# Performance work log

Measured on AMD Instinct MI355X. Metric: run time of the kernel, lower is better.

Reference implementation:

```python
import jax, jax.numpy as jnp
import numpy as np

EMBED = 768
HIDDEN = 3072
HEADS = 12
EPS = 1e-6


def _ln(x, g, b):
    mu = jnp.mean(x, axis=-1, keepdims=True)
    var = jnp.mean(jnp.square(x - mu), axis=-1, keepdims=True)
    return (x - mu) / jnp.sqrt(var + EPS) * g + b


def setup_inputs() -> dict:
    key = jax.random.key(0)
    ks = jax.random.split(key, 12)
    s = lambda fan_in: 1.0 / np.sqrt(fan_in)
    x = jax.random.normal(ks[0], (16, 1024, EMBED), dtype=jnp.float32)
    return {
        "x": x,
        "ln1_g": jnp.ones((EMBED,), jnp.float32),
        "ln1_b": jnp.zeros((EMBED,), jnp.float32),
        "qkv_w": jax.random.uniform(ks[1], (3 * EMBED, EMBED), jnp.float32, -s(EMBED), s(EMBED)),
        "qkv_b": jax.random.uniform(ks[2], (3 * EMBED,), jnp.float32, -s(EMBED), s(EMBED)),
        "proj_w": jax.random.uniform(ks[3], (EMBED, EMBED), jnp.float32, -s(EMBED), s(EMBED)),
        "proj_b": jax.random.uniform(ks[4], (EMBED,), jnp.float32, -s(EMBED), s(EMBED)),
        "ln2_g": jnp.ones((EMBED,), jnp.float32),
        "ln2_b": jnp.zeros((EMBED,), jnp.float32),
        "fc1_w": jax.random.uniform(ks[5], (HIDDEN, EMBED), jnp.float32, -s(EMBED), s(EMBED)),
        "fc1_b": jax.random.uniform(ks[6], (HIDDEN,), jnp.float32, -s(EMBED), s(EMBED)),
        "fc2_w": jax.random.uniform(ks[7], (EMBED, HIDDEN), jnp.float32, -s(HIDDEN), s(HIDDEN)),
        "fc2_b": jax.random.uniform(ks[8], (EMBED,), jnp.float32, -s(HIDDEN), s(HIDDEN)),
    }


def reference(x, ln1_g, ln1_b, qkv_w, qkv_b, proj_w, proj_b, ln2_g, ln2_b, fc1_w, fc1_b, fc2_w, fc2_b):
    B, N, D = x.shape
    Hd = D // HEADS
    scale = Hd ** -0.5
    # attention branch
    xn = _ln(x, ln1_g, ln1_b)
    qkv = xn @ qkv_w.T + qkv_b  # [B,N,3D]
    qkv = qkv.reshape(B, N, 3, HEADS, Hd).transpose(2, 0, 3, 1, 4)
    q, k, v = qkv[0], qkv[1], qkv[2]  # [B,H,N,Hd]
    attn = jax.nn.softmax(jnp.einsum("bhqd,bhkd->bhqk", q, k) * scale, axis=-1)
    ctx = jnp.einsum("bhqk,bhkd->bhqd", attn, v)
    ctx = ctx.transpose(0, 2, 1, 3).reshape(B, N, D)
    x = x + ctx @ proj_w.T + proj_b
    # MLP branch
    h = _ln(x, ln2_g, ln2_b)
    h = jax.nn.gelu(h @ fc1_w.T + fc1_b, approximate=False)
    x = x + h @ fc2_w.T + fc2_b
    return x
```

## Files before the change

kernel.cpp:

```cpp
#include <hip/hip_runtime.h>
#include <math.h>


typedef unsigned short u16;
typedef __attribute__((ext_vector_type(8))) short bf16x8;
typedef __attribute__((ext_vector_type(4))) float f32x4;

#define MFMA_BF16(a, b, c) __builtin_amdgcn_mfma_f32_16x16x32_bf16((a), (b), (c), 0, 0, 0)
#define WAITV(N) asm volatile("s_waitcnt vmcnt(" #N ")" ::: "memory")
#define WAITLGKM0 asm volatile("s_waitcnt lgkmcnt(0)" ::: "memory")
#define SCHED0 __builtin_amdgcn_sched_barrier(0)
#define EXP2F(x) __builtin_amdgcn_exp2f(x)

#define QSCALE 0.18033688011112042f
#define C8LOG2E 11.541560327111707f

__device__ __forceinline__ float bf2f(u16 v) {
    return __uint_as_float(((unsigned)v) << 16);
}
__device__ __forceinline__ u16 f2bf(float f) {
    unsigned u = __float_as_uint(f);
    u += 0x7fffu + ((u >> 16) & 1u);
    return (u16)(u >> 16);
}
__device__ __forceinline__ unsigned cvtpk_bf16(float lo, float hi) {
    unsigned r;
    asm volatile("v_cvt_pk_bf16_f32 %0, %1, %2" : "=v"(r) : "v"(lo), "v"(hi));
    return r;
}

__device__ __forceinline__ float gelu_fast(float v) {
    const float t = v * v;
    const float z = v * (1.5957691216f + 0.0713548162f * t);
    const float e = __expf(-z);
    return v * __builtin_amdgcn_rcpf(1.0f + e);
}

typedef __attribute__((address_space(1))) const void gvoid;
typedef __attribute__((address_space(3))) void lvoid;
__device__ __forceinline__ void gll16(const void* g, void* l) {
    __builtin_amdgcn_global_load_lds((gvoid*)g, (lvoid*)l, 16, 0, 0);
}

__global__ __launch_bounds__(256) void cast32(const float* __restrict__ src,
                                              u16* __restrict__ dst, int n8) {
    const int i = blockIdx.x * 256 + threadIdx.x;
    if (i >= n8) return;
    const float4 a = ((const float4*)src)[2 * i];
    const float4 b = ((const float4*)src)[2 * i + 1];
    bf16x8 r;
    r[0] = (short)f2bf(a.x); r[1] = (short)f2bf(a.y);
    r[2] = (short)f2bf(a.z); r[3] = (short)f2bf(a.w);
    r[4] = (short)f2bf(b.x); r[5] = (short)f2bf(b.y);
    r[6] = (short)f2bf(b.z); r[7] = (short)f2bf(b.w);
    ((bf16x8*)dst)[i] = r;
}

__global__ __launch_bounds__(256) void ln_kernel(const float* __restrict__ x,
                                                 const float* __restrict__ g,
                                                 const float* __restrict__ b,
                                                 u16* __restrict__ out) {
    const int row = blockIdx.x;
    const int t = threadIdx.x;
    const float* xr = x + (size_t)row * 768;
    float v0 = xr[t], v1 = xr[t + 256], v2 = xr[t + 512];
    float s = v0 + v1 + v2;
    float sq = v0 * v0 + v1 * v1 + v2 * v2;
#pragma unroll
    for (int off = 32; off > 0; off >>= 1) {
        s += __shfl_down(s, off);
        sq += __shfl_down(sq, off);
    }
    __shared__ float red_s[4], red_sq[4], sh_mu, sh_rs;
    const int wave = t >> 6, lane = t & 63;
    if (lane == 0) { red_s[wave] = s; red_sq[wave] = sq; }
    __syncthreads();
    if (t == 0) {
        float S = red_s[0] + red_s[1] + red_s[2] + red_s[3];
        float SQ = red_sq[0] + red_sq[1] + red_sq[2] + red_sq[3];
        float mu = S * (1.0f / 768.0f);
        float var = SQ * (1.0f / 768.0f) - mu * mu;
        sh_mu = mu;
        sh_rs = 1.0f / sqrtf(fmaxf(var, 0.0f) + 1e-6f);
    }
    __syncthreads();
    const float mu = sh_mu, rs = sh_rs;
    u16* orow = out + (size_t)row * 768;
    orow[t]       = f2bf((v0 - mu) * rs * g[t]       + b[t]);
    orow[t + 256] = f2bf((v1 - mu) * rs * g[t + 256] + b[t + 256]);
    orow[t + 512] = f2bf((v2 - mu) * rs * g[t + 512] + b[t + 512]);
}

template <int EPI, int BF16B>
__global__ __launch_bounds__(256, 2) void gemm2(
        const u16* __restrict__ A, const void* __restrict__ Bv,
        const float* __restrict__ bias, const float* __restrict__ res,
        void* __restrict__ Cv, u16* __restrict__ vtb, int N, int K) {
    __shared__ __align__(16) u16 As[128 * 32];
    __shared__ __align__(16) u16 Bs[128 * 32];
    const int t = threadIdx.x;
    const int wave = t >> 6, lane = t & 63;
    const int quad = lane >> 4, mr = lane & 15;
    const int wm = wave >> 1, wn = wave & 1;
    const int m0 = blockIdx.y * 128;
    const int n0 = blockIdx.x * 128;

    f32x4 acc[4][4];
#pragma unroll
    for (int i = 0; i < 4; i++)
#pragma unroll
        for (int j = 0; j < 4; j++) acc[i][j] = (f32x4){0.f, 0.f, 0.f, 0.f};

    const int seg = wave * 2;
    const int drow = lane >> 2;
    const int dcol = (lane & 3) * 8;
    const int sr = t >> 2, skv = t & 3;

    for (int k0 = 0; k0 < K; k0 += 32) {
#pragma unroll
        for (int c = 0; c < 2; c++) {
            const int rowA = (seg + c) * 16 + drow;
            gll16(A + (size_t)(m0 + rowA) * K + k0 + dcol, &As[(seg + c) * 512]);
        }
        if (BF16B) {
            const u16* Bh = (const u16*)Bv;
#pragma unroll
            for (int c = 0; c < 2; c++) {
                const int rowB = (seg + c) * 16 + drow;
                gll16(Bh + (size_t)(n0 + rowB) * K + k0 + dcol, &Bs[(seg + c) * 512]);
            }
        } else {
            const float* Bf = (const float*)Bv;
#pragma unroll
            for (int half = 0; half < 2; half++) {
                const float* src = Bf + (size_t)(n0 + sr + half * 64) * K + k0 + skv * 8;
                const float4 a = *(const float4*)src;
                const float4 b2 = *(const float4*)(src + 4);
                bf16x8 r;
                r[0] = (short)f2bf(a.x);  r[1] = (short)f2bf(a.y);
                r[2] = (short)f2bf(a.z);  r[3] = (short)f2bf(a.w);
                r[4] = (short)f2bf(b2.x); r[5] = (short)f2bf(b2.y);
                r[6] = (short)f2bf(b2.z); r[7] = (short)f2bf(b2.w);
                *(bf16x8*)&Bs[(sr + half * 64) * 32 + skv * 8] = r;
            }
        }
        __syncthreads();
        bf16x8 af[4], bfr[4];
#pragma unroll
        for (int i = 0; i < 4; i++)
            af[i] = *(const bf16x8*)&As[(wm * 64 + i * 16 + mr) * 32 + quad * 8];
#pragma unroll
        for (int j = 0; j < 4; j++)
            bfr[j] = *(const bf16x8*)&Bs[(wn * 64 + j * 16 + mr) * 32 + quad * 8];
#pragma unroll
        for (int i = 0; i < 4; i++)
#pragma unroll
            for (int j = 0; j < 4; j++)
                acc[i][j] = MFMA_BF16(af[i], bfr[j], acc[i][j]);
        __syncthreads();
    }

#pragma unroll
    for (int i = 0; i < 4; i++) {
#pragma unroll
        for (int r = 0; r < 4; r++) {
            const int m = m0 + wm * 64 + i * 16 + quad * 4 + r;
#pragma unroll
            for (int j = 0; j < 4; j++) {
                const int n = n0 + wn * 64 + j * 16 + mr;
                float v = acc[i][j][r] + bias[n];
                if (EPI == 1) {
                    v = gelu_fast(v);
                    ((u16*)Cv)[(size_t)m * N + n] = f2bf(v);
                } else if (EPI == 2) {
                    v += res[(size_t)m * N + n];
                    ((float*)Cv)[(size_t)m * N + n] = v;
                } else {
                    if (n < 1536) {
                        const float vq = (n < 768) ? v * QSCALE : v;
                        ((u16*)Cv)[(size_t)m * 1536 + n] = f2bf(vq);
                    } else {
                        const int h = (n - 1536) >> 6, hd = (n - 1536) & 63;
                        const int bb = m >> 10, pos = m & 1023;
                        vtb[((size_t)(bb * 12 + h) * 64 + hd) * 1024 + pos] = f2bf(v);
                    }
                }
            }
        }
    }
}

#define AFRAG(T, ROW, KS) \
    (*(const bf16x8*)&(T)[(ROW)][(((((KS) << 2) | quad)) ^ ((ROW) & 7)) << 3])

#define ACCUM(ACCEL, AF, BF)                                  \
    do {                                                      \
        if (EPI == 3) (ACCEL) = MFMA_BF16((AF), (BF), (ACCEL)); \
        else          (ACCEL) = MFMA_BF16((BF), (AF), (ACCEL)); \
    } while (0)

template <int EPI, int NSLOT>
__global__ __launch_bounds__(512, 2) void gemm8(
        const u16* __restrict__ A, const u16* __restrict__ Bw,
        const float* __restrict__ bias, const float* __restrict__ res,
        void* __restrict__ Cv, u16* __restrict__ vtb, int N, int K) {
    constexpr int TN = NSLOT * 64;
    __shared__ __align__(16) u16 SMEM[(512 + 2 * TN) * 64];
    u16(&As)[2][256][64] = *reinterpret_cast<u16(*)[2][256][64]>(&SMEM[0]);
    u16(&Bs)[2][TN][64] = *reinterpret_cast<u16(*)[2][TN][64]>(&SMEM[512 * 64]);
    const int t = threadIdx.x;
    const int wave = t >> 6, lane = t & 63;
    const int quad = lane >> 4, mr = lane & 15;
    const int wm = wave >> 2, wn = wave & 3;
    const int gx = gridDim.x;
    const int nwg = gx * gridDim.y;
    int bid = blockIdx.y * gx + blockIdx.x;
    bid = (bid & 7) * (nwg >> 3) + (bid >> 3);
    const int m0 = (bid / gx) * 256, n0 = (bid % gx) * TN;
    const int NT = K >> 6;

    const int srow = wave * 8 + (lane >> 3);
    const int sgrp = ((lane & 7) ^ (lane >> 3)) * 8;

    const u16* Abase = A + (size_t)(m0 + srow) * K + sgrp;
    const u16* Bbase = Bw + (size_t)(n0 + srow) * K + sgrp;

#define STAGE_A(BI, SLOT, KT) \
    gll16(Abase + ((size_t)(SLOT) * 64) * K + (KT) * 64, &As[BI][(SLOT) * 64 + wave * 8][0])
#define STAGE_B(BI, SLOT, KT) \
    gll16(Bbase + ((size_t)(SLOT) * 64) * K + (KT) * 64, &Bs[BI][(SLOT) * 64 + wave * 8][0])

    STAGE_A(0, 0, 0); STAGE_A(0, 1, 0); STAGE_A(0, 2, 0); STAGE_A(0, 3, 0);
#pragma unroll
    for (int s = 0; s < NSLOT; s++) STAGE_B(0, s, 0);
    if (NT > 1) { STAGE_A(1, 0, 1); STAGE_A(1, 2, 1); STAGE_B(1, 0, 1); STAGE_B(1, 1, 1); }

    f32x4 acc[8][NSLOT];
#pragma unroll
    for (int i = 0; i < 8; i++)
#pragma unroll
        for (int j = 0; j < NSLOT; j++) acc[i][j] = (f32x4){0.f, 0.f, 0.f, 0.f};

    if (NT > 1) { WAITV(4); } else { WAITV(0); }
    __builtin_amdgcn_s_barrier();
    SCHED0;

    for (int kt = 0; kt < NT; ++kt) {
        const int bi = kt & 1;
        const u16(*Ab)[64] = As[bi];
        const u16(*Bb)[64] = Bs[bi];
        const bool st1 = (kt + 1 < NT);
        const bool st2 = (kt + 2 < NT);

        if (st1) {
#pragma unroll
            for (int s = 2; s < NSLOT; s++) STAGE_B(bi ^ 1, s, kt + 1);
            STAGE_A(bi ^ 1, 1, kt + 1); STAGE_A(bi ^ 1, 3, kt + 1);
        }

        bf16x8 af[4], bfv[NSLOT];
#pragma unroll
        for (int j = 0; j < NSLOT; j++) bfv[j] = AFRAG(Bb, wn * (NSLOT * 16) + j * 16 + mr, 0);
#pragma unroll
        for (int i = 0; i < 4; i++) af[i] = AFRAG(Ab, wm * 128 + i * 16 + mr, 0);
#pragma unroll
        for (int i = 0; i < 4; i++)
#pragma unroll
            for (int j = 0; j < NSLOT; j++) ACCUM(acc[i][j], af[i], bfv[j]);
#pragma unroll
        for (int i = 0; i < 4; i++) af[i] = AFRAG(Ab, wm * 128 + 64 + i * 16 + mr, 0);
#pragma unroll
        for (int i = 0; i < 4; i++)
#pragma unroll
            for (int j = 0; j < NSLOT; j++) ACCUM(acc[4 + i][j], af[i], bfv[j]);
#pragma unroll
        for (int j = 0; j < NSLOT; j++) bfv[j] = AFRAG(Bb, wn * (NSLOT * 16) + j * 16 + mr, 1);
#pragma unroll
        for (int i = 0; i < 4; i++) af[i] = AFRAG(Ab, wm * 128 + i * 16 + mr, 1);
#pragma unroll
        for (int i = 0; i < 4; i++)
#pragma unroll
            for (int j = 0; j < NSLOT; j++) ACCUM(acc[i][j], af[i], bfv[j]);
#pragma unroll
        for (int i = 0; i < 4; i++) af[i] = AFRAG(Ab, wm * 128 + 64 + i * 16 + mr, 1);
#pragma unroll
        for (int i = 0; i < 4; i++)
#pragma unroll
            for (int j = 0; j < NSLOT; j++) ACCUM(acc[4 + i][j], af[i], bfv[j]);

        WAITLGKM0;
        SCHED0;
        __builtin_amdgcn_s_barrier();
        SCHED0;
        if (st2) { STAGE_A(bi, 0, kt + 2); STAGE_A(bi, 2, kt + 2);
                   STAGE_B(bi, 0, kt + 2); STAGE_B(bi, 1, kt + 2); }
        SCHED0;
        if (st2) { WAITV(4); } else { WAITV(0); }
        __builtin_amdgcn_s_barrier();
        SCHED0;
    }

    if (EPI == 3) {
        if (n0 >= 1536) {
            u16* Ls = &SMEM[0];
            __syncthreads();
#pragma unroll
            for (int i = 0; i < 8; i++) {
                const int mbase = wm * 128 + (i >> 2) * 64 + (i & 3) * 16 + quad * 4;
                const int mch = mbase >> 3, mlo = mbase & 7;
#pragma unroll
                for (int j = 0; j < NSLOT; j++) {
                    const int nl = wn * (NSLOT * 16) + j * 16 + mr;
                    float v0 = acc[i][j][0] + bias[n0 + nl];
                    float v1 = acc[i][j][1] + bias[n0 + nl];
                    float v2 = acc[i][j][2] + bias[n0 + nl];
                    float v3 = acc[i][j][3] + bias[n0 + nl];
                    ushort4 w;
                    w.x = f2bf(v0); w.y = f2bf(v1); w.z = f2bf(v2); w.w = f2bf(v3);
                    *(ushort4*)(Ls + nl * 256 + ((mch ^ (nl & 7)) << 3) + mlo) = w;
                }
            }
            __syncthreads();
            const int bb = m0 >> 10, pos0 = m0 & 1023;
#pragma unroll
            for (int it = 0; it < TN / 8; it++) {
                const int nl = it * 8 + wave;
                const int h = (n0 - 1536 + nl) >> 6;
                const int hd = nl & 63;
                const int mch = (lane >> 1) ^ (nl & 7);
                const ushort4 v =
                    *(const ushort4*)(Ls + nl * 256 + (mch << 3) + (lane & 1) * 4);
                u16* dst = vtb + ((size_t)(bb * 12 + h) * 64 + hd) * 1024 + pos0 + lane * 4;
                *(ushort4*)dst = v;
            }
        } else {
#pragma unroll
            for (int i = 0; i < 8; i++) {
#pragma unroll
                for (int r = 0; r < 4; r++) {
                    const int m = m0 + wm * 128 + (i >> 2) * 64 + (i & 3) * 16 + quad * 4 + r;
#pragma unroll
                    for (int j = 0; j < NSLOT; j++) {
                        const int n = n0 + wn * (NSLOT * 16) + j * 16 + mr;
                        float v = acc[i][j][r] + bias[n];
                        const float vq = (n < 768) ? v * QSCALE : v;
                        ((u16*)Cv)[(size_t)m * 1536 + n] = f2bf(vq);
                    }
                }
            }
        }
    } else {
#pragma unroll
        for (int ii = 0; ii < 8; ii++) {
            const int m = m0 + wm * 128 + (ii >> 2) * 64 + (ii & 3) * 16 + mr;
#pragma unroll
            for (int j = 0; j < NSLOT; j++) {
                const int n = n0 + wn * (NSLOT * 16) + j * 16 + quad * 4;
                const float4 b4 = *(const float4*)&bias[n];
                const float v0 = acc[ii][j][0] + b4.x;
                const float v1 = acc[ii][j][1] + b4.y;
                const float v2 = acc[ii][j][2] + b4.z;
                const float v3 = acc[ii][j][3] + b4.w;
                if (EPI == 1) {
                    ushort4 w;
                    w.x = f2bf(gelu_fast(v0)); w.y = f2bf(gelu_fast(v1));
                    w.z = f2bf(gelu_fast(v2)); w.w = f2bf(gelu_fast(v3));
                    *(ushort4*)&((u16*)Cv)[(size_t)m * N + n] = w;
                } else {
                    const float4 r4 = *(const float4*)&res[(size_t)m * N + n];
                    float4 o;
                    o.x = v0 + r4.x; o.y = v1 + r4.y; o.z = v2 + r4.z; o.w = v3 + r4.w;
                    *(float4*)&((float*)Cv)[(size_t)m * N + n] = o;
                }
            }
        }
    }
#undef STAGE_A
#undef STAGE_B
}

__global__ __launch_bounds__(512) void attn2(const u16* __restrict__ qkkb,
                                             const u16* __restrict__ vtb,
                                             u16* __restrict__ ctx) {
    __shared__ __align__(16) u16 Ks[2][64][72];
    __shared__ __align__(16) u16 Vt[2][64][72];
    __shared__ __align__(16) u16 Ps[128][72];
    const int L = blockIdx.y * gridDim.x + blockIdx.x;
    const int lxcd = L & 7, li = L >> 3;
    const int bh = lxcd * 24 + (li >> 3);
    const int q0 = (li & 7) * 128;
    const int b = bh / 12, h = bh % 12;
    const int t = threadIdx.x;
    const int wave = t >> 6, lane = t & 63, quad = lane >> 4, mr = lane & 15;

    const u16* qrow = qkkb + (size_t)(b * 1024 + q0 + wave * 16 + mr) * 1536 + h * 64;
    const bf16x8 qf0 = *(const bf16x8*)(qrow + quad * 8);
    const bf16x8 qf1 = *(const bf16x8*)(qrow + 32 + quad * 8);

    const u16* kbase = qkkb + (size_t)b * 1024 * 1536 + 768 + h * 64;
    const u16* vbase = vtb + (size_t)bh * 64 * 1024;

    const int srow = t >> 3;
    const int sv = t & 7;

    f32x4 oacc[4];
#pragma unroll
    for (int j = 0; j < 4; j++) oacc[j] = (f32x4){0.f, 0.f, 0.f, 0.f};
    float lsum = 0.f;

    bf16x8 pk0, pv0;
    pk0 = *(const bf16x8*)(kbase + (size_t)srow * 1536 + sv * 8);
    pv0 = *(const bf16x8*)(vbase + (size_t)srow * 1024 + sv * 8);
    *(bf16x8*)&Ks[0][srow][sv * 8] = pk0;
    *(bf16x8*)&Vt[0][srow][sv * 8] = pv0;

    for (int kt = 0; kt < 16; ++kt) {
        __syncthreads();
        const int cur = kt & 1;
        if (kt < 15) {
            const size_t ko = (size_t)(kt + 1) * 64;
            pk0 = *(const bf16x8*)(kbase + (ko + srow) * 1536 + sv * 8);
            pv0 = *(const bf16x8*)(vbase + (size_t)srow * 1024 + ko + sv * 8);
        }
        f32x4 sf[4];
#pragma unroll
        for (int j = 0; j < 4; j++) {
            const bf16x8 kf0 = *(const bf16x8*)&Ks[cur][j * 16 + mr][quad * 8];
            const bf16x8 kf1 = *(const bf16x8*)&Ks[cur][j * 16 + mr][32 + quad * 8];
            f32x4 s = (f32x4){0.f, 0.f, 0.f, 0.f};
            s = MFMA_BF16(kf0, qf0, s);
            s = MFMA_BF16(kf1, qf1, s);
            sf[j] = s;
        }
#pragma unroll
        for (int j = 0; j < 4; j++) {
            const float p0 = EXP2F(sf[j][0] - C8LOG2E);
            const float p1 = EXP2F(sf[j][1] - C8LOG2E);
            const float p2 = EXP2F(sf[j][2] - C8LOG2E);
            const float p3 = EXP2F(sf[j][3] - C8LOG2E);
            lsum += (p0 + p1) + (p2 + p3);
            uint2 w;
            w.x = cvtpk_bf16(p0, p1);
            w.y = cvtpk_bf16(p2, p3);
            *(uint2*)&Ps[wave * 16 + mr][j * 16 + quad * 4] = w;
        }
        __asm__ __volatile__("s_waitcnt lgkmcnt(0)" ::: "memory");
#pragma unroll
        for (int st = 0; st < 2; st++) {
            const bf16x8 pf = *(const bf16x8*)&Ps[wave * 16 + mr][st * 32 + quad * 8];
#pragma unroll
            for (int j = 0; j < 4; j++) {
                const bf16x8 vf = *(const bf16x8*)&Vt[cur][j * 16 + mr][st * 32 + quad * 8];
                oacc[j] = MFMA_BF16(vf, pf, oacc[j]);
            }
        }
        if (kt < 15) {
            const int nxt = cur ^ 1;
            *(bf16x8*)&Ks[nxt][srow][sv * 8] = pk0;
            *(bf16x8*)&Vt[nxt][srow][sv * 8] = pv0;
        }
    }

    lsum += __shfl_xor(lsum, 16);
    lsum += __shfl_xor(lsum, 32);
    const float inv = 1.0f / lsum;
    u16* dst = ctx + (size_t)(b * 1024 + q0 + wave * 16 + mr) * 768 + h * 64;
#pragma unroll
    for (int j = 0; j < 4; j++) {
        ushort4 w;
        w.x = f2bf(oacc[j][0] * inv);
        w.y = f2bf(oacc[j][1] * inv);
        w.z = f2bf(oacc[j][2] * inv);
        w.w = f2bf(oacc[j][3] * inv);
        *(ushort4*)(dst + j * 16 + quad * 4) = w;
    }
}

extern "C" void kernel_launch(void* const* d_in, const int* in_sizes, int n_in,
                              void* d_out, int out_size, void* d_ws, size_t ws_size,
                              hipStream_t stream) {
    const float* x      = (const float*)d_in[0];
    const float* ln1_g  = (const float*)d_in[1];
    const float* ln1_b  = (const float*)d_in[2];
    const float* qkv_w  = (const float*)d_in[3];
    const float* qkv_b  = (const float*)d_in[4];
    const float* proj_w = (const float*)d_in[5];
    const float* proj_b = (const float*)d_in[6];
    const float* ln2_g  = (const float*)d_in[7];
    const float* ln2_b  = (const float*)d_in[8];
    const float* fc1_w  = (const float*)d_in[9];
    const float* fc1_b  = (const float*)d_in[10];
    const float* fc2_w  = (const float*)d_in[11];
    const float* fc2_b  = (const float*)d_in[12];
    float* out = (float*)d_out;

    char* base = (char*)d_ws + 1024;
    u16* xn   = (u16*)base;
    u16* qkkb = (u16*)(base + 25165824);
    u16* vtb  = (u16*)(base + 75497472);
    u16* h1   = (u16*)(base + 25165824);
    u16* ctxb = xn;
    u16* hn   = xn;

    const size_t WOFF = 125830144ull;
    const bool big = ws_size >= 139985920ull;
    u16* wqkv  = (u16*)((char*)d_ws + WOFF);
    u16* wproj = (u16*)((char*)d_ws + WOFF + 3538944);
    u16* wfc1  = (u16*)((char*)d_ws + WOFF + 4718592);
    u16* wfc2  = (u16*)((char*)d_ws + WOFF + 9437184);

    if (big) {
        cast32<<<dim3(864),  dim3(256), 0, stream>>>(qkv_w,  wqkv,  221184);
        cast32<<<dim3(288),  dim3(256), 0, stream>>>(proj_w, wproj, 73728);
        cast32<<<dim3(1152), dim3(256), 0, stream>>>(fc1_w,  wfc1,  294912);
        cast32<<<dim3(1152), dim3(256), 0, stream>>>(fc2_w,  wfc2,  294912);
    }

    ln_kernel<<<dim3(16384), dim3(256), 0, stream>>>(x, ln1_g, ln1_b, xn);

    if (big)
        gemm8<3, 3><<<dim3(12, 64), dim3(512), 0, stream>>>(
            xn, wqkv, qkv_b, nullptr, qkkb, vtb, 2304, 768);
    else
        gemm2<3, 0><<<dim3(18, 128), dim3(256), 0, stream>>>(
            xn, qkv_w, qkv_b, nullptr, qkkb, vtb, 2304, 768);

    attn2<<<dim3(8, 192), dim3(512), 0, stream>>>(qkkb, vtb, ctxb);

    if (big)
        gemm8<2, 3><<<dim3(4, 64), dim3(512), 0, stream>>>(
            ctxb, wproj, proj_b, x, out, nullptr, 768, 768);
    else
        gemm2<2, 0><<<dim3(6, 128), dim3(256), 0, stream>>>(
            ctxb, proj_w, proj_b, x, out, nullptr, 768, 768);

    ln_kernel<<<dim3(16384), dim3(256), 0, stream>>>(out, ln2_g, ln2_b, hn);

    if (big)
        gemm8<1, 4><<<dim3(12, 64), dim3(512), 0, stream>>>(
            hn, wfc1, fc1_b, nullptr, h1, nullptr, 3072, 768);
    else
        gemm2<1, 0><<<dim3(24, 128), dim3(256), 0, stream>>>(
            hn, fc1_w, fc1_b, nullptr, h1, nullptr, 3072, 768);

    if (big)
        gemm8<2, 3><<<dim3(4, 64), dim3(512), 0, stream>>>(
            h1, wfc2, fc2_b, out, out, nullptr, 768, 3072);
    else
        gemm2<2, 0><<<dim3(6, 128), dim3(256), 0, stream>>>(
            h1, fc2_w, fc2_b, out, out, nullptr, 768, 3072);
}
```

Before: 504.8 us.

## Run GEMM tiles with 16 waves per block and simple double buffering

Moves the GEMM kernel from 8 waves of 512 threads to 16 waves of 1024 threads per block. Each wave now owns a 64-row slice instead of 128 rows, so accumulator registers are halved. The staggered half-tile prefetch with partial vmcnt waits is replaced by plain double buffering that waits for all loads each iteration. The aim is more latency hiding from extra waves and lower register pressure, at the cost of one block per CU and a coarser pipeline. The wave-to-row mapping (wm, wn, srow) and the staging-slot coverage must match the new 16-wave layout, and that code is not fully visible here.

Result: no change. 505.7 us (+0.2%).

```diff
diff --git a/kernel.cpp b/kernel.cpp
--- a/kernel.cpp
+++ b/kernel.cpp
@@ -7,7 +7,7 @@
 typedef __attribute__((ext_vector_type(4))) float f32x4;
 
 #define MFMA_BF16(a, b, c) __builtin_amdgcn_mfma_f32_16x16x32_bf16((a), (b), (c), 0, 0, 0)
-#define WAITV(N) asm volatile("s_waitcnt vmcnt(" #N ")" ::: "memory")
+#define WAITV0 asm volatile("s_waitcnt vmcnt(0)" ::: "memory")
 #define WAITLGKM0 asm volatile("s_waitcnt lgkmcnt(0)" ::: "memory")
 #define SCHED0 __builtin_amdgcn_sched_barrier(0)
 #define EXP2F(x) __builtin_amdgcn_exp2f(x)
@@ -200,7 +200,7 @@
     } while (0)
 
 template <int EPI, int NSLOT>
-__global__ __launch_bounds__(512, 2) void gemm8(
+__global__ __launch_bounds__(1024) void gemm16(
         const u16* __restrict__ A, const u16* __restrict__ Bw,
         const float* __restrict__ bias, const float* __restrict__ res,
         void* __restrict__ Cv, u16* __restrict__ vtb, int N, int K) {
@@ -225,23 +225,27 @@
     const u16* Abase = A + (size_t)(m0 + srow) * K + sgrp;
     const u16* Bbase = Bw + (size_t)(n0 + srow) * K + sgrp;
 
-#define STAGE_A(BI, SLOT, KT) \
-    gll16(Abase + ((size_t)(SLOT) * 64) * K + (KT) * 64, &As[BI][(SLOT) * 64 + wave * 8][0])
-#define STAGE_B(BI, SLOT, KT) \
-    gll16(Bbase + ((size_t)(SLOT) * 64) * K + (KT) * 64, &Bs[BI][(SLOT) * 64 + wave * 8][0])
-
-    STAGE_A(0, 0, 0); STAGE_A(0, 1, 0); STAGE_A(0, 2, 0); STAGE_A(0, 3, 0);
-#pragma unroll
-    for (int s = 0; s < NSLOT; s++) STAGE_B(0, s, 0);
-    if (NT > 1) { STAGE_A(1, 0, 1); STAGE_A(1, 2, 1); STAGE_B(1, 0, 1); STAGE_B(1, 1, 1); }
-
-    f32x4 acc[8][NSLOT];
-#pragma unroll
-    for (int i = 0; i < 8; i++)
+#define STAGE_A16(BI, U, KT) \
+    gll16(Abase + ((size_t)(U) * 128) * K + (KT) * 64, &As[BI][(U) * 128 + wave * 8][0])
+#define STAGE_B16(BI, KT)                                                          \
+    do {                                                                           \
+        gll16(Bbase + (size_t)(KT) * 64, &Bs[BI][wave * 8][0]);                    \
+        if (TN == 256) {                                                           \
+            gll16(Bbase + (size_t)128 * K + (KT) * 64, &Bs[BI][128 + wave * 8][0]);\
+        } else if (wave < 8) {                                                     \
+            gll16(Bbase + (size_t)128 * K + (KT) * 64, &Bs[BI][128 + wave * 8][0]);\
+        }                                                                          \
+    } while (0)
+
+    STAGE_A16(0, 0, 0); STAGE_A16(0, 1, 0); STAGE_B16(0, 0);
+
+    f32x4 acc[4][NSLOT];
+#pragma unroll
+    for (int i = 0; i < 4; i++)
 #pragma unroll
         for (int j = 0; j < NSLOT; j++) acc[i][j] = (f32x4){0.f, 0.f, 0.f, 0.f};
 
-    if (NT > 1) { WAITV(4); } else { WAITV(0); }
+    WAITV0;
     __builtin_amdgcn_s_barrier();
     SCHED0;
 
@@ -249,53 +253,31 @@
         const int bi = kt & 1;
         const u16(*Ab)[64] = As[bi];
         const u16(*Bb)[64] = Bs[bi];
-        const bool st1 = (kt + 1 < NT);
-        const bool st2 = (kt + 2 < NT);
-
-        if (st1) {
-#pragma unroll
-            for (int s = 2; s < NSLOT; s++) STAGE_B(bi ^ 1, s, kt + 1);
-            STAGE_A(bi ^ 1, 1, kt + 1); STAGE_A(bi ^ 1, 3, kt + 1);
-        }
-
-        bf16x8 af[4], bfv[NSLOT];
-#pragma unroll
-        for (int j = 0; j < NSLOT; j++) bfv[j] = AFRAG(Bb, wn * (NSLOT * 16) + j * 16 + mr, 0);
-#pragma unroll
-        for (int i = 0; i < 4; i++) af[i] = AFRAG(Ab, wm * 128 + i * 16 + mr, 0);
-#pragma unroll
-        for (int i = 0; i < 4; i++)
-#pragma unroll
-            for (int j = 0; j < NSLOT; j++) ACCUM(acc[i][j], af[i], bfv[j]);
-#pragma unroll
-        for (int i = 0; i < 4; i++) af[i] = AFRAG(Ab, wm * 128 + 64 + i * 16 + mr, 0);
-#pragma unroll
-        for (int i = 0; i < 4; i++)
-#pragma unroll
-            for (int j = 0; j < NSLOT; j++) ACCUM(acc[4 + i][j], af[i], bfv[j]);
-#pragma unroll
-        for (int j = 0; j < NSLOT; j++) bfv[j] = AFRAG(Bb, wn * (NSLOT * 16) + j * 16 + mr, 1);
-#pragma unroll
-        for (int i = 0; i < 4; i++) af[i] = AFRAG(Ab, wm * 128 + i * 16 + mr, 1);
-#pragma unroll
-        for (int i = 0; i < 4; i++)
-#pragma unroll
-            for (int j = 0; j < NSLOT; j++) ACCUM(acc[i][j], af[i], bfv[j]);
-#pragma unroll
-        for (int i = 0; i < 4; i++) af[i] = AFRAG(Ab, wm * 128 + 64 + i * 16 + mr, 1);
-#pragma unroll
-        for (int i = 0; i < 4; i++)
-#pragma unroll
-            for (int j = 0; j < NSLOT; j++) ACCUM(acc[4 + i][j], af[i], bfv[j]);
+
+        if (kt + 1 < NT) {
+            STAGE_A16(bi ^ 1, 0, kt + 1);
+            STAGE_A16(bi ^ 1, 1, kt + 1);
+            STAGE_B16(bi ^ 1, kt + 1);
+        }
+
+        bf16x8 af[4], bf[NSLOT];
+#pragma unroll
+        for (int ks = 0; ks < 2; ks++) {
+#pragma unroll
+            for (int j = 0; j < NSLOT; j++)
+                bf[j] = AFRAG(Bb, wn * (NSLOT * 16) + j * 16 + mr, ks);
+#pragma unroll
+            for (int i = 0; i < 4; i++)
+                af[i] = AFRAG(Ab, wm * 64 + i * 16 + mr, ks);
+#pragma unroll
+            for (int i = 0; i < 4; i++)
+#pragma unroll
+                for (int j = 0; j < NSLOT; j++) ACCUM(acc[i][j], af[i], bf[j]);
+        }
 
         WAITLGKM0;
         SCHED0;
-        __builtin_amdgcn_s_barrier();
-        SCHED0;
-        if (st2) { STAGE_A(bi, 0, kt + 2); STAGE_A(bi, 2, kt + 2);
-                   STAGE_B(bi, 0, kt + 2); STAGE_B(bi, 1, kt + 2); }
-        SCHED0;
-        if (st2) { WAITV(4); } else { WAITV(0); }
+        WAITV0;
         __builtin_amdgcn_s_barrier();
         SCHED0;
     }
@@ -305,8 +287,8 @@
             u16* Ls = &SMEM[0];
             __syncthreads();
 #pragma unroll
-            for (int i = 0; i < 8; i++) {
-                const int mbase = wm * 128 + (i >> 2) * 64 + (i & 3) * 16 + quad * 4;
+            for (int i = 0; i < 4; i++) {
+                const int mbase = wm * 64 + i * 16 + quad * 4;
                 const int mch = mbase >> 3, mlo = mbase & 7;
 #pragma unroll
                 for (int j = 0; j < NSLOT; j++) {
@@ -323,8 +305,8 @@
             __syncthreads();
             const int bb = m0 >> 10, pos0 = m0 & 1023;
 #pragma unroll
-            for (int it = 0; it < TN / 8; it++) {
-                const int nl = it * 8 + wave;
+            for (int it2 = 0; it2 < TN / 16; it2++) {
+                const int nl = it2 * 16 + wave;
                 const int h = (n0 - 1536 + nl) >> 6;
                 const int hd = nl & 63;
                 const int mch = (lane >> 1) ^ (nl & 7);
@@ -335,10 +317,10 @@
             }
         } else {
 #pragma unroll
-            for (int i = 0; i < 8; i++) {
+            for (int i = 0; i < 4; i++) {
 #pragma unroll
                 for (int r = 0; r < 4; r++) {
-                    const int m = m0 + wm * 128 + (i >> 2) * 64 + (i & 3) * 16 + quad * 4 + r;
+                    const int m = m0 + wm * 64 + i * 16 + quad * 4 + r;
 #pragma unroll
                     for (int j = 0; j < NSLOT; j++) {
                         const int n = n0 + wn * (NSLOT * 16) + j * 16 + mr;
@@ -351,8 +333,8 @@
         }
     } else {
 #pragma unroll
-        for (int ii = 0; ii < 8; ii++) {
-            const int m = m0 + wm * 128 + (ii >> 2) * 64 + (ii & 3) * 16 + mr;
+        for (int ii = 0; ii < 4; ii++) {
+            const int m = m0 + wm * 64 + ii * 16 + mr;
 #pragma unroll
             for (int j = 0; j < NSLOT; j++) {
                 const int n = n0 + wn * (NSLOT * 16) + j * 16 + quad * 4;
@@ -375,8 +357,8 @@
             }
         }
     }
-#undef STAGE_A
-#undef STAGE_B
+#undef STAGE_A16
+#undef STAGE_B16
 }
 
 __global__ __launch_bounds__(512) void attn2(const u16* __restrict__ qkkb,
@@ -519,7 +501,7 @@
     ln_kernel<<<dim3(16384), dim3(256), 0, stream>>>(x, ln1_g, ln1_b, xn);
 
     if (big)
-        gemm8<3, 3><<<dim3(12, 64), dim3(512), 0, stream>>>(
+        gemm16<3, 3><<<dim3(12, 64), dim3(1024), 0, stream>>>(
             xn, wqkv, qkv_b, nullptr, qkkb, vtb, 2304, 768);
     else
         gemm2<3, 0><<<dim3(18, 128), dim3(256), 0, stream>>>(
@@ -528,7 +510,7 @@
     attn2<<<dim3(8, 192), dim3(512), 0, stream>>>(qkkb, vtb, ctxb);
 
     if (big)
-        gemm8<2, 3><<<dim3(4, 64), dim3(512), 0, stream>>>(
+        gemm16<2, 3><<<dim3(4, 64), dim3(1024), 0, stream>>>(
             ctxb, wproj, proj_b, x, out, nullptr, 768, 768);
     else
         gemm2<2, 0><<<dim3(6, 128), dim3(256), 0, stream>>>(
@@ -537,14 +519,14 @@
     ln_kernel<<<dim3(16384), dim3(256), 0, stream>>>(out, ln2_g, ln2_b, hn);
 
     if (big)
-        gemm8<1, 4><<<dim3(12, 64), dim3(512), 0, stream>>>(
+        gemm16<1, 4><<<dim3(12, 64), dim3(1024), 0, stream>>>(
             hn, wfc1, fc1_b, nullptr, h1, nullptr, 3072, 768);
     else
         gemm2<1, 0><<<dim3(24, 128), dim3(256), 0, stream>>>(
             hn, fc1_w, fc1_b, nullptr, h1, nullptr, 3072, 768);
 
     if (big)
-        gemm8<2, 3><<<dim3(4, 64), dim3(512), 0, stream>>>(
+        gemm16<2, 3><<<dim3(4, 64), dim3(1024), 0, stream>>>(
             h1, wfc2, fc2_b, out, out, nullptr, 768, 3072);
     else
         gemm2<2, 0><<<dim3(6, 128), dim3(256), 0, stream>>>(
```
